# Kernel optimization log

Measured on AMD Instinct MI355X. Metric: run time of the kernel, lower is better.

The kernel has to match this reference:

```python
import jax, jax.numpy as jnp
import numpy as np

P = 0.5  # dropout fraction (init kwarg p)


def setup_inputs() -> dict:
    key = jax.random.key(0)
    # positive weights (e.g. post-softmax attention), shape [B, M, N]
    w = jax.random.uniform(key, (8192, 1, 4096), dtype=jnp.float32, minval=1e-4, maxval=1.0)
    return {"w": w}


def reference(w) -> jnp.ndarray:
    # Drop the bottom int(N*P) entries along dim 2 (per row), then renormalize
    # the surviving entries with a softmax over them; dropped entries stay 0.
    B, M, N = w.shape
    k = int(N * P)  # number of smallest entries zeroed per row
    if k == 0:
        return w
    order = jnp.argsort(w, axis=2)          # ascending order indices
    ranks = jnp.argsort(order, axis=2)      # rank of each element in its row
    keep = ranks >= k                        # True for the top (N-k) entries
    neg = jnp.finfo(w.dtype).min
    logits = jnp.where(keep, w, neg)
    m = jnp.max(logits, axis=2, keepdims=True)
    e = jnp.where(keep, jnp.exp(logits - m), 0.0)
    return e / jnp.sum(e, axis=2, keepdims=True)
```

## Files before the change

kernel.cpp:

```cpp
#include <hip/hip_runtime.h>
#include <stdint.h>

constexpr int N     = 4096;
constexpr int KSEL  = 2048;
constexpr int BLOCK = 256;
constexpr int NW    = BLOCK / 64;
constexpr int EPT   = N / BLOCK;
constexpr int NB    = 256;
constexpr int CAP   = 128;
constexpr float P1  = 0.45f;
constexpr float P2  = 0.55f;
constexpr float BSCALE = 2560.0f;

typedef float vfloat4 __attribute__((ext_vector_type(4)));

__global__ __launch_bounds__(BLOCK, 8)
void wdrop_kernel(const float* __restrict__ w, float* __restrict__ out) {
    const int t = threadIdx.x, wid = t >> 6, lane = t & 63;
    const uint64_t row = blockIdx.x;

    __shared__ alignas(16) int hist[NB];
    __shared__ uint32_t redu[NW];
    __shared__ int      redi[NW];
    __shared__ float    redf[NW];
    __shared__ int      selb, selc, cn;
    __shared__ uint32_t cb[CAP];
    __shared__ int      ci[CAP];
    __shared__ uint32_t thrT, thrI;

    uint32_t v[EPT];
    {
        const uint4* wf = (const uint4*)(w + row * N);
        uint4 u[EPT / 4];
#pragma unroll
        for (int j = 0; j < EPT / 4; ++j) u[j] = wf[j * BLOCK + t];
#pragma unroll
        for (int j = 0; j < EPT / 4; ++j) {
            v[j*4+0] = u[j].x; v[j*4+1] = u[j].y;
            v[j*4+2] = u[j].z; v[j*4+3] = u[j].w;
        }
    }
    hist[t] = 0;
    if (t == 0) cn = 0;

    uint32_t mx = v[0];
    int clo = 0, chi = 0;
#pragma unroll
    for (int e = 0; e < EPT; ++e) {
        mx = max(mx, v[e]);
        const float f = __uint_as_float(v[e]);
        clo += (f < P1); chi += (f < P2);
    }
    int pk = (clo << 16) | chi;
#pragma unroll
    for (int off = 32; off > 0; off >>= 1) {
        mx = max(mx, (uint32_t)__shfl_xor((int)mx, off, 64));
        pk += __shfl_xor(pk, off, 64);
    }
    if (lane == 0) { redu[wid] = mx; redi[wid] = pk; }
    __syncthreads();

#pragma unroll
    for (int e = 0; e < EPT; ++e) {
        const float f = __uint_as_float(v[e]);
        if (f >= P1 && f < P2) {
            const int bk = min((int)((f - P1) * BSCALE), NB - 1);
            atomicAdd(&hist[bk], 1);
        }
    }
    uint32_t mxb = redu[0]; int pkt = redi[0];
#pragma unroll
    for (int i = 1; i < NW; ++i) { mxb = max(mxb, redu[i]); pkt += redi[i]; }
    const int cloB = pkt >> 16, chiB = pkt & 0xFFFF;
    const bool fastp = (cloB < KSEL) && (chiB >= KSEL);
    const int jrank = KSEL - cloB;
    __syncthreads();

    if (wid == 0) {
        const int4 hh = ((const int4*)hist)[lane];
        const int a0 = hh.x, a1 = a0 + hh.y, a2 = a1 + hh.z, a3 = a2 + hh.w;
        int sc = a3;
#pragma unroll
        for (int off = 1; off < 64; off <<= 1) {
            const int u = __shfl_up(sc, off, 64);
            if (lane >= off) sc += u;
        }
        const int base = sc - a3;
        if (fastp) {
            const int inc[4] = {base + a0, base + a1, base + a2, base + a3};
            const int exc[4] = {base, base + a0, base + a1, base + a2};
#pragma unroll
            for (int i = 0; i < 4; ++i)
                if (exc[i] < jrank && jrank <= inc[i]) { selb = lane * 4 + i; selc = exc[i]; }
        }
    }
    __syncthreads();

    if (fastp) {
        const int bs = selb;
#pragma unroll
        for (int e = 0; e < EPT; ++e) {
            const float f = __uint_as_float(v[e]);
            if (f >= P1 && f < P2 && min((int)((f - P1) * BSCALE), NB - 1) == bs) {
                const int slot = atomicAdd(&cn, 1);
                if (slot < CAP) {
                    cb[slot] = v[e];
                    ci[slot] = ((e >> 2) * BLOCK + t) * 4 + (e & 3);
                }
            }
        }
    }
    __syncthreads();

    const bool ok = fastp && (cn <= CAP);
    if (ok && t < cn) {
        const uint32_t myb = cb[t]; const int myi = ci[t];
        const int cc = cn;
        int rank = 0;
        for (int q = 0; q < cc; ++q)
            rank += (cb[q] < myb) || (cb[q] == myb && ci[q] < myi);
        if (rank == jrank - selc - 1) { thrT = myb; thrI = (uint32_t)myi; }
    }

    if (!ok) {
        uint32_t blo = 0u, bhi = 0x7f7fffffu;
        while (blo < bhi) {
            const uint32_t mid = blo + ((bhi - blo) >> 1);
            int c = 0;
#pragma unroll
            for (int e = 0; e < EPT; ++e) c += __popcll(__ballot(v[e] <= mid));
            __syncthreads();
            if (lane == 0) redi[wid] = c;
            __syncthreads();
            int tot = 0;
#pragma unroll
            for (int i = 0; i < NW; ++i) tot += redi[i];
            if (tot >= KSEL) bhi = mid; else blo = mid + 1;
        }
        const uint32_t T = blo;
        int c = 0;
#pragma unroll
        for (int e = 0; e < EPT; ++e) c += __popcll(__ballot(v[e] < T));
        __syncthreads();
        if (lane == 0) redi[wid] = c;
        __syncthreads();
        int clt = 0;
#pragma unroll
        for (int i = 0; i < NW; ++i) clt += redi[i];
        const int need = KSEL - clt;
        int ilo = 0, ihi = N - 1;
        while (ilo < ihi) {
            const int imid = (ilo + ihi) >> 1;
            int cc2 = 0;
#pragma unroll
            for (int e = 0; e < EPT; ++e) {
                const int idx = ((e >> 2) * BLOCK + t) * 4 + (e & 3);
                cc2 += __popcll(__ballot(v[e] == T && idx <= imid));
            }
            __syncthreads();
            if (lane == 0) redi[wid] = cc2;
            __syncthreads();
            int tot = 0;
#pragma unroll
            for (int i = 0; i < NW; ++i) tot += redi[i];
            if (tot >= need) ihi = imid; else ilo = imid + 1;
        }
        if (t == 0) { thrT = T; thrI = (uint32_t)ilo; }
    }
    __syncthreads();

    const uint32_t T = thrT; const int ti = (int)thrI;
    const float m = __uint_as_float(mxb);
    float acc = 0.0f;
#pragma unroll
    for (int e = 0; e < EPT; ++e) {
        const int idx = ((e >> 2) * BLOCK + t) * 4 + (e & 3);
        const bool keep = (v[e] > T) || (v[e] == T && idx > ti);
        const float ev = keep ? __expf(__uint_as_float(v[e]) - m) : 0.0f;
        v[e] = __float_as_uint(ev);
        acc += ev;
    }
#pragma unroll
    for (int off = 32; off > 0; off >>= 1) acc += __shfl_xor(acc, off, 64);
    if (lane == 0) redf[wid] = acc;
    __syncthreads();
    float s = redf[0];
#pragma unroll
    for (int i = 1; i < NW; ++i) s += redf[i];
    const float inv = 1.0f / s;

    vfloat4* of = (vfloat4*)(out + row * N);
#pragma unroll
    for (int j = 0; j < EPT / 4; ++j) {
        vfloat4 o;
        o.x = __uint_as_float(v[j*4+0]) * inv;
        o.y = __uint_as_float(v[j*4+1]) * inv;
        o.z = __uint_as_float(v[j*4+2]) * inv;
        o.w = __uint_as_float(v[j*4+3]) * inv;
        __builtin_nontemporal_store(o, &of[j * BLOCK + t]);
    }
}

extern "C" void kernel_launch(void* const* d_in, const int* in_sizes, int n_in,
                              void* d_out, int out_size, void* d_ws, size_t ws_size,
                              hipStream_t stream) {
    const float* w = (const float*)d_in[0];
    float* out = (float*)d_out;
    const int rows = in_sizes[0] / N;
    wdrop_kernel<<<rows, BLOCK, 0, stream>>>(w, out);
}
```

Baseline: 232.0 us.

## Map one row per wavefront and drop block-level synchronisation

Each wavefront now processes a whole row with 64 elements per lane, using per-wave histograms, ballot-based candidate compaction and shuffle reductions instead of block-wide barriers and shared reductions. The max pass is removed and exp is applied to raw values, relying on softmax shift invariance. This removes barrier and shared-memory reduction overhead, at the cost of higher register pressure, lower occupancy and overflow risk for large inputs.

```diff
diff --git a/kernel.cpp b/kernel.cpp
--- a/kernel.cpp
+++ b/kernel.cpp
@@ -4,200 +4,174 @@
 constexpr int N     = 4096;
 constexpr int KSEL  = 2048;
 constexpr int BLOCK = 256;
-constexpr int NW    = BLOCK / 64;
-constexpr int EPT   = N / BLOCK;
+constexpr int NWAVE = BLOCK / 64;
+constexpr int EPL   = 64;
 constexpr int NB    = 256;
-constexpr int CAP   = 128;
+constexpr int CAP   = 64;
 constexpr float P1  = 0.45f;
 constexpr float P2  = 0.55f;
 constexpr float BSCALE = 2560.0f;
 
 typedef float vfloat4 __attribute__((ext_vector_type(4)));
 
-__global__ __launch_bounds__(BLOCK, 8)
+__global__ __launch_bounds__(BLOCK, 4)
 void wdrop_kernel(const float* __restrict__ w, float* __restrict__ out) {
     const int t = threadIdx.x, wid = t >> 6, lane = t & 63;
-    const uint64_t row = blockIdx.x;
+    const uint64_t row = (uint64_t)blockIdx.x * NWAVE + wid;
 
-    __shared__ alignas(16) int hist[NB];
-    __shared__ uint32_t redu[NW];
-    __shared__ int      redi[NW];
-    __shared__ float    redf[NW];
-    __shared__ int      selb, selc, cn;
-    __shared__ uint32_t cb[CAP];
-    __shared__ int      ci[CAP];
-    __shared__ uint32_t thrT, thrI;
+    __shared__ alignas(16) int hist[NWAVE][NB];
+    __shared__ uint32_t cb[NWAVE][CAP];
+    __shared__ int      ci[NWAVE][CAP];
 
-    uint32_t v[EPT];
+    uint32_t v[EPL];
     {
         const uint4* wf = (const uint4*)(w + row * N);
-        uint4 u[EPT / 4];
+        uint4 u[16];
 #pragma unroll
-        for (int j = 0; j < EPT / 4; ++j) u[j] = wf[j * BLOCK + t];
+        for (int j = 0; j < 16; ++j) u[j] = wf[j * 64 + lane];
 #pragma unroll
-        for (int j = 0; j < EPT / 4; ++j) {
+        for (int j = 0; j < 16; ++j) {
             v[j*4+0] = u[j].x; v[j*4+1] = u[j].y;
             v[j*4+2] = u[j].z; v[j*4+3] = u[j].w;
         }
     }
-    hist[t] = 0;
-    if (t == 0) cn = 0;
 
-    uint32_t mx = v[0];
-    int clo = 0, chi = 0;
+    ((int4*)hist[wid])[lane] = int4{0, 0, 0, 0};
+    __threadfence_block();
+
+    int clo = 0;
 #pragma unroll
-    for (int e = 0; e < EPT; ++e) {
-        mx = max(mx, v[e]);
+    for (int e = 0; e < EPL; ++e) {
         const float f = __uint_as_float(v[e]);
-        clo += (f < P1); chi += (f < P2);
+        clo += (f < P1);
+        if (f >= P1 && f < P2)
+            atomicAdd(&hist[wid][min((int)((f - P1) * BSCALE), NB - 1)], 1);
     }
-    int pk = (clo << 16) | chi;
 #pragma unroll
-    for (int off = 32; off > 0; off >>= 1) {
-        mx = max(mx, (uint32_t)__shfl_xor((int)mx, off, 64));
-        pk += __shfl_xor(pk, off, 64);
+    for (int off = 32; off > 0; off >>= 1) clo += __shfl_xor(clo, off, 64);
+    __threadfence_block();
+
+    const int4 hh = ((const int4*)hist[wid])[lane];
+    const int a0 = hh.x, a1 = a0 + hh.y, a2 = a1 + hh.z, a3 = a2 + hh.w;
+    int sc = a3;
+#pragma unroll
+    for (int off = 1; off < 64; off <<= 1) {
+        const int u = __shfl_up(sc, off, 64);
+        if (lane >= off) sc += u;
     }
-    if (lane == 0) { redu[wid] = mx; redi[wid] = pk; }
-    __syncthreads();
+    const int base = sc - a3;
+    const int tot  = __shfl(sc, 63, 64);
+    bool fastp = (clo < KSEL) && (clo + tot >= KSEL);
+    int selb = -1, jms = 0;
+    if (fastp) {
+        const int jrank = KSEL - clo;
+        const int inc[4] = {base + a0, base + a1, base + a2, base + a3};
+        const int exc[4] = {base, base + a0, base + a1, base + a2};
+#pragma unroll
+        for (int i = 0; i < 4; ++i)
+            if (exc[i] < jrank && jrank <= inc[i]) {
+                selb = lane * 4 + i;
+                jms  = jrank - exc[i] - 1;
+            }
+        const unsigned long long b = __ballot(selb >= 0);
+        const int src = __ffsll((unsigned long long)b) - 1;
+        selb = __shfl(selb, src, 64);
+        jms  = __shfl(jms,  src, 64);
+    }
 
+    uint32_t thrT = 0; int thrI = 0;
+    if (fastp) {
+        int cn = 0;
 #pragma unroll
-    for (int e = 0; e < EPT; ++e) {
-        const float f = __uint_as_float(v[e]);
-        if (f >= P1 && f < P2) {
-            const int bk = min((int)((f - P1) * BSCALE), NB - 1);
-            atomicAdd(&hist[bk], 1);
+        for (int e = 0; e < EPL; ++e) {
+            const float f = __uint_as_float(v[e]);
+            const bool in = (f >= P1) && (f < P2) &&
+                            (min((int)((f - P1) * BSCALE), NB - 1) == selb);
+            const unsigned long long m = __ballot(in);
+            if (in) {
+                const int slot = cn + __popcll(m & ((1ull << lane) - 1ull));
+                if (slot < CAP) {
+                    cb[wid][slot] = v[e];
+                    ci[wid][slot] = ((e >> 2) * 64 + lane) * 4 + (e & 3);
+                }
+            }
+            cn += __popcll(m);
+        }
+        if (cn > CAP) fastp = false;
+        if (fastp) {
+            __threadfence_block();
+            bool found = false; uint32_t myT = 0; int myI = 0;
+            if (lane < cn) {
+                const uint32_t myb = cb[wid][lane]; const int myi = ci[wid][lane];
+                int rank = 0;
+                for (int q = 0; q < cn; ++q)
+                    rank += (cb[wid][q] < myb) ||
+                            (cb[wid][q] == myb && ci[wid][q] < myi);
+                if (rank == jms) { found = true; myT = myb; myI = myi; }
+            }
+            const unsigned long long b = __ballot(found);
+            const int src = __ffsll((unsigned long long)b) - 1;
+            thrT = (uint32_t)__shfl((int)myT, src, 64);
+            thrI = __shfl(myI, src, 64);
         }
     }
-    uint32_t mxb = redu[0]; int pkt = redi[0];
-#pragma unroll
-    for (int i = 1; i < NW; ++i) { mxb = max(mxb, redu[i]); pkt += redi[i]; }
-    const int cloB = pkt >> 16, chiB = pkt & 0xFFFF;
-    const bool fastp = (cloB < KSEL) && (chiB >= KSEL);
-    const int jrank = KSEL - cloB;
-    __syncthreads();
 
-    if (wid == 0) {
-        const int4 hh = ((const int4*)hist)[lane];
-        const int a0 = hh.x, a1 = a0 + hh.y, a2 = a1 + hh.z, a3 = a2 + hh.w;
-        int sc = a3;
-#pragma unroll
-        for (int off = 1; off < 64; off <<= 1) {
-            const int u = __shfl_up(sc, off, 64);
-            if (lane >= off) sc += u;
-        }
-        const int base = sc - a3;
-        if (fastp) {
-            const int inc[4] = {base + a0, base + a1, base + a2, base + a3};
-            const int exc[4] = {base, base + a0, base + a1, base + a2};
-#pragma unroll
-            for (int i = 0; i < 4; ++i)
-                if (exc[i] < jrank && jrank <= inc[i]) { selb = lane * 4 + i; selc = exc[i]; }
-        }
-    }
-    __syncthreads();
-
-    if (fastp) {
-        const int bs = selb;
-#pragma unroll
-        for (int e = 0; e < EPT; ++e) {
-            const float f = __uint_as_float(v[e]);
-            if (f >= P1 && f < P2 && min((int)((f - P1) * BSCALE), NB - 1) == bs) {
-                const int slot = atomicAdd(&cn, 1);
-                if (slot < CAP) {
-                    cb[slot] = v[e];
-                    ci[slot] = ((e >> 2) * BLOCK + t) * 4 + (e & 3);
-                }
-            }
-        }
-    }
-    __syncthreads();
-
-    const bool ok = fastp && (cn <= CAP);
-    if (ok && t < cn) {
-        const uint32_t myb = cb[t]; const int myi = ci[t];
-        const int cc = cn;
-        int rank = 0;
-        for (int q = 0; q < cc; ++q)
-            rank += (cb[q] < myb) || (cb[q] == myb && ci[q] < myi);
-        if (rank == jrank - selc - 1) { thrT = myb; thrI = (uint32_t)myi; }
-    }
-
-    if (!ok) {
+    if (!fastp) {
         uint32_t blo = 0u, bhi = 0x7f7fffffu;
         while (blo < bhi) {
             const uint32_t mid = blo + ((bhi - blo) >> 1);
             int c = 0;
 #pragma unroll
-            for (int e = 0; e < EPT; ++e) c += __popcll(__ballot(v[e] <= mid));
-            __syncthreads();
-            if (lane == 0) redi[wid] = c;
-            __syncthreads();
-            int tot = 0;
+            for (int e = 0; e < EPL; ++e) c += (v[e] <= mid);
 #pragma unroll
-            for (int i = 0; i < NW; ++i) tot += redi[i];
-            if (tot >= KSEL) bhi = mid; else blo = mid + 1;
+            for (int off = 32; off > 0; off >>= 1) c += __shfl_xor(c, off, 64);
+            if (c >= KSEL) bhi = mid; else blo = mid + 1;
         }
         const uint32_t T = blo;
         int c = 0;
 #pragma unroll
-        for (int e = 0; e < EPT; ++e) c += __popcll(__ballot(v[e] < T));
-        __syncthreads();
-        if (lane == 0) redi[wid] = c;
-        __syncthreads();
-        int clt = 0;
+        for (int e = 0; e < EPL; ++e) c += (v[e] < T);
 #pragma unroll
-        for (int i = 0; i < NW; ++i) clt += redi[i];
-        const int need = KSEL - clt;
+        for (int off = 32; off > 0; off >>= 1) c += __shfl_xor(c, off, 64);
+        const int need = KSEL - c;
         int ilo = 0, ihi = N - 1;
         while (ilo < ihi) {
             const int imid = (ilo + ihi) >> 1;
-            int cc2 = 0;
+            int cc = 0;
 #pragma unroll
-            for (int e = 0; e < EPT; ++e) {
-                const int idx = ((e >> 2) * BLOCK + t) * 4 + (e & 3);
-                cc2 += __popcll(__ballot(v[e] == T && idx <= imid));
+            for (int e = 0; e < EPL; ++e) {
+                const int idx = ((e >> 2) * 64 + lane) * 4 + (e & 3);
+                cc += (v[e] == T && idx <= imid);
             }
-            __syncthreads();
-            if (lane == 0) redi[wid] = cc2;
-            __syncthreads();
-            int tot = 0;
 #pragma unroll
-            for (int i = 0; i < NW; ++i) tot += redi[i];
-            if (tot >= need) ihi = imid; else ilo = imid + 1;
+            for (int off = 32; off > 0; off >>= 1) cc += __shfl_xor(cc, off, 64);
+            if (cc >= need) ihi = imid; else ilo = imid + 1;
         }
-        if (t == 0) { thrT = T; thrI = (uint32_t)ilo; }
+        thrT = T; thrI = ilo;
     }
-    __syncthreads();
 
-    const uint32_t T = thrT; const int ti = (int)thrI;
-    const float m = __uint_as_float(mxb);
     float acc = 0.0f;
 #pragma unroll
-    for (int e = 0; e < EPT; ++e) {
-        const int idx = ((e >> 2) * BLOCK + t) * 4 + (e & 3);
-        const bool keep = (v[e] > T) || (v[e] == T && idx > ti);
-        const float ev = keep ? __expf(__uint_as_float(v[e]) - m) : 0.0f;
+    for (int e = 0; e < EPL; ++e) {
+        const int idx = ((e >> 2) * 64 + lane) * 4 + (e & 3);
+        const bool keep = (v[e] > thrT) || (v[e] == thrT && idx > thrI);
+        const float ev = keep ? __expf(__uint_as_float(v[e])) : 0.0f;
         v[e] = __float_as_uint(ev);
         acc += ev;
     }
 #pragma unroll
     for (int off = 32; off > 0; off >>= 1) acc += __shfl_xor(acc, off, 64);
-    if (lane == 0) redf[wid] = acc;
-    __syncthreads();
-    float s = redf[0];
-#pragma unroll
-    for (int i = 1; i < NW; ++i) s += redf[i];
-    const float inv = 1.0f / s;
+    const float inv = 1.0f / acc;
 
     vfloat4* of = (vfloat4*)(out + row * N);
 #pragma unroll
-    for (int j = 0; j < EPT / 4; ++j) {
+    for (int j = 0; j < 16; ++j) {
         vfloat4 o;
         o.x = __uint_as_float(v[j*4+0]) * inv;
         o.y = __uint_as_float(v[j*4+1]) * inv;
         o.z = __uint_as_float(v[j*4+2]) * inv;
         o.w = __uint_as_float(v[j*4+3]) * inv;
-        __builtin_nontemporal_store(o, &of[j * BLOCK + t]);
+        __builtin_nontemporal_store(o, &of[j * 64 + lane]);
     }
 }
 
@@ -207,5 +181,5 @@
     const float* w = (const float*)d_in[0];
     float* out = (float*)d_out;
     const int rows = in_sizes[0] / N;
-    wdrop_kernel<<<rows, BLOCK, 0, stream>>>(w, out);
+    wdrop_kernel<<<rows / NWAVE, BLOCK, 0, stream>>>(w, out);
 }
```

Result: slower. 241.1 us (+3.9%).

## Single-pass per-wave histogram and candidate pool, drop max reduction

Applied to the files above, without the earlier changes.

Replaces the two-pass selection (global histogram, then a second scan of registers for the selected bucket) with a single pass. Each wave builds its own histogram and a pool of mid-range values with their indices. Wave 0 then finds the threshold bucket, compacts candidates from the pools with ballots, and ranks them, which removes several block-wide barriers. The row-max reduction is also dropped: exp is applied directly to the weights, which relies on inputs being at most 1 so that exp cannot overflow. The fallback path now uses shuffle reductions instead of ballots.

```diff
diff --git a/kernel.cpp b/kernel.cpp
--- a/kernel.cpp
+++ b/kernel.cpp
@@ -5,12 +5,13 @@
 constexpr int KSEL  = 2048;
 constexpr int BLOCK = 256;
 constexpr int NW    = BLOCK / 64;
-constexpr int EPT   = N / BLOCK;
-constexpr int NB    = 256;
-constexpr int CAP   = 128;
+constexpr int EPT   = 16;
+constexpr int NB    = 64;
+constexpr int PCAP  = 160;
+constexpr int CCAP  = 48;
 constexpr float P1  = 0.45f;
 constexpr float P2  = 0.55f;
-constexpr float BSCALE = 2560.0f;
+constexpr float BSCALE = 640.0f;
 
 typedef float vfloat4 __attribute__((ext_vector_type(4)));
 
@@ -19,164 +20,168 @@
     const int t = threadIdx.x, wid = t >> 6, lane = t & 63;
     const uint64_t row = blockIdx.x;
 
-    __shared__ alignas(16) int hist[NB];
-    __shared__ uint32_t redu[NW];
+    __shared__ int      hist[NW][NB];
+    __shared__ int      pcnt[NW];
+    __shared__ uint2    pool[NW][PCAP];
+    __shared__ int      wclo[NW];
     __shared__ int      redi[NW];
     __shared__ float    redf[NW];
-    __shared__ int      selb, selc, cn;
-    __shared__ uint32_t cb[CAP];
-    __shared__ int      ci[CAP];
-    __shared__ uint32_t thrT, thrI;
+    __shared__ uint32_t candB[CCAP];
+    __shared__ int      candI[CCAP];
+    __shared__ uint32_t bT, bI;
+    __shared__ int      bFlag;
 
     uint32_t v[EPT];
     {
         const uint4* wf = (const uint4*)(w + row * N);
-        uint4 u[EPT / 4];
-#pragma unroll
-        for (int j = 0; j < EPT / 4; ++j) u[j] = wf[j * BLOCK + t];
-#pragma unroll
-        for (int j = 0; j < EPT / 4; ++j) {
+        uint4 u[4];
+#pragma unroll
+        for (int j = 0; j < 4; ++j) u[j] = wf[j * BLOCK + t];
+#pragma unroll
+        for (int j = 0; j < 4; ++j) {
             v[j*4+0] = u[j].x; v[j*4+1] = u[j].y;
             v[j*4+2] = u[j].z; v[j*4+3] = u[j].w;
         }
     }
-    hist[t] = 0;
-    if (t == 0) cn = 0;
-
-    uint32_t mx = v[0];
-    int clo = 0, chi = 0;
-#pragma unroll
-    for (int e = 0; e < EPT; ++e) {
-        mx = max(mx, v[e]);
-        const float f = __uint_as_float(v[e]);
-        clo += (f < P1); chi += (f < P2);
-    }
-    int pk = (clo << 16) | chi;
-#pragma unroll
-    for (int off = 32; off > 0; off >>= 1) {
-        mx = max(mx, (uint32_t)__shfl_xor((int)mx, off, 64));
-        pk += __shfl_xor(pk, off, 64);
-    }
-    if (lane == 0) { redu[wid] = mx; redi[wid] = pk; }
-    __syncthreads();
-
+
+    hist[wid][lane] = 0;
+    if (lane == 0) pcnt[wid] = 0;
+    __threadfence_block();
+
+    int clo = 0;
 #pragma unroll
     for (int e = 0; e < EPT; ++e) {
         const float f = __uint_as_float(v[e]);
-        if (f >= P1 && f < P2) {
+        if (f < P1) {
+            ++clo;
+        } else if (f < P2) {
             const int bk = min((int)((f - P1) * BSCALE), NB - 1);
-            atomicAdd(&hist[bk], 1);
-        }
-    }
-    uint32_t mxb = redu[0]; int pkt = redi[0];
-#pragma unroll
-    for (int i = 1; i < NW; ++i) { mxb = max(mxb, redu[i]); pkt += redi[i]; }
-    const int cloB = pkt >> 16, chiB = pkt & 0xFFFF;
-    const bool fastp = (cloB < KSEL) && (chiB >= KSEL);
-    const int jrank = KSEL - cloB;
+            atomicAdd(&hist[wid][bk], 1);
+            const int slot = atomicAdd(&pcnt[wid], 1);
+            if (slot < PCAP)
+                pool[wid][slot] = make_uint2(
+                    v[e], (uint32_t)(((e >> 2) * BLOCK + t) * 4 + (e & 3)));
+        }
+    }
+#pragma unroll
+    for (int off = 32; off > 0; off >>= 1) clo += __shfl_xor(clo, off, 64);
+    if (lane == 0) wclo[wid] = clo;
     __syncthreads();
 
     if (wid == 0) {
-        const int4 hh = ((const int4*)hist)[lane];
-        const int a0 = hh.x, a1 = a0 + hh.y, a2 = a1 + hh.z, a3 = a2 + hh.w;
-        int sc = a3;
+        const int cloB = wclo[0] + wclo[1] + wclo[2] + wclo[3];
+        const int h = hist[0][lane] + hist[1][lane] + hist[2][lane] + hist[3][lane];
+        int sc = h;
 #pragma unroll
         for (int off = 1; off < 64; off <<= 1) {
             const int u = __shfl_up(sc, off, 64);
             if (lane >= off) sc += u;
         }
-        const int base = sc - a3;
-        if (fastp) {
-            const int inc[4] = {base + a0, base + a1, base + a2, base + a3};
-            const int exc[4] = {base, base + a0, base + a1, base + a2};
-#pragma unroll
-            for (int i = 0; i < 4; ++i)
-                if (exc[i] < jrank && jrank <= inc[i]) { selb = lane * 4 + i; selc = exc[i]; }
-        }
-    }
-    __syncthreads();
-
-    if (fastp) {
-        const int bs = selb;
-#pragma unroll
-        for (int e = 0; e < EPT; ++e) {
-            const float f = __uint_as_float(v[e]);
-            if (f >= P1 && f < P2 && min((int)((f - P1) * BSCALE), NB - 1) == bs) {
-                const int slot = atomicAdd(&cn, 1);
-                if (slot < CAP) {
-                    cb[slot] = v[e];
-                    ci[slot] = ((e >> 2) * BLOCK + t) * 4 + (e & 3);
+        const int tot = __shfl(sc, 63, 64);
+        bool ok = (cloB < KSEL) && (cloB + tot >= KSEL) &&
+                  (pcnt[0] <= PCAP) && (pcnt[1] <= PCAP) &&
+                  (pcnt[2] <= PCAP) && (pcnt[3] <= PCAP);
+        int selb = -1, jms = 0;
+        if (ok) {
+            const int jrank = KSEL - cloB;
+            const int exc = sc - h;
+            const bool hit = (exc < jrank) && (jrank <= sc);
+            const unsigned long long bb = __ballot(hit);
+            const int src = __ffsll(bb) - 1;
+            selb = __shfl(lane, src, 64);
+            jms  = __shfl(jrank - exc - 1, src, 64);
+        }
+        int cn = 0;
+        if (ok) {
+#pragma unroll
+            for (int wv = 0; wv < NW; ++wv) {
+                const int pn = pcnt[wv];
+                for (int k = 0; k < pn; k += 64) {
+                    const int id = k + lane;
+                    bool in = false; uint2 pe = make_uint2(0u, 0u);
+                    if (id < pn) {
+                        pe = pool[wv][id];
+                        const float pf = __uint_as_float(pe.x);
+                        in = (min((int)((pf - P1) * BSCALE), NB - 1) == selb);
+                    }
+                    const unsigned long long m = __ballot(in);
+                    if (in) {
+                        const int slot = cn + __popcll(m & ((1ull << lane) - 1ull));
+                        if (slot < CCAP) { candB[slot] = pe.x; candI[slot] = (int)pe.y; }
+                    }
+                    cn += __popcll(m);
                 }
             }
-        }
+            if (cn > CCAP) ok = false;
+        }
+        if (ok) {
+            __threadfence_block();
+            if (lane < cn) {
+                const uint32_t myb = candB[lane]; const int myi = candI[lane];
+                int rank = 0;
+                for (int q = 0; q < cn; ++q)
+                    rank += (candB[q] < myb) || (candB[q] == myb && candI[q] < myi);
+                if (rank == jms) { bT = myb; bI = (uint32_t)myi; }
+            }
+        }
+        if (lane == 0) bFlag = ok ? 0 : 1;
     }
     __syncthreads();
 
-    const bool ok = fastp && (cn <= CAP);
-    if (ok && t < cn) {
-        const uint32_t myb = cb[t]; const int myi = ci[t];
-        const int cc = cn;
-        int rank = 0;
-        for (int q = 0; q < cc; ++q)
-            rank += (cb[q] < myb) || (cb[q] == myb && ci[q] < myi);
-        if (rank == jrank - selc - 1) { thrT = myb; thrI = (uint32_t)myi; }
-    }
-
-    if (!ok) {
+    if (bFlag) {
         uint32_t blo = 0u, bhi = 0x7f7fffffu;
         while (blo < bhi) {
             const uint32_t mid = blo + ((bhi - blo) >> 1);
             int c = 0;
 #pragma unroll
-            for (int e = 0; e < EPT; ++e) c += __popcll(__ballot(v[e] <= mid));
-            __syncthreads();
+            for (int e = 0; e < EPT; ++e) c += (v[e] <= mid);
+#pragma unroll
+            for (int off = 32; off > 0; off >>= 1) c += __shfl_xor(c, off, 64);
             if (lane == 0) redi[wid] = c;
             __syncthreads();
-            int tot = 0;
-#pragma unroll
-            for (int i = 0; i < NW; ++i) tot += redi[i];
+            const int tot = redi[0] + redi[1] + redi[2] + redi[3];
+            __syncthreads();
             if (tot >= KSEL) bhi = mid; else blo = mid + 1;
         }
         const uint32_t T = blo;
         int c = 0;
 #pragma unroll
-        for (int e = 0; e < EPT; ++e) c += __popcll(__ballot(v[e] < T));
-        __syncthreads();
+        for (int e = 0; e < EPT; ++e) c += (v[e] < T);
+#pragma unroll
+        for (int off = 32; off > 0; off >>= 1) c += __shfl_xor(c, off, 64);
         if (lane == 0) redi[wid] = c;
         __syncthreads();
-        int clt = 0;
-#pragma unroll
-        for (int i = 0; i < NW; ++i) clt += redi[i];
+        const int clt = redi[0] + redi[1] + redi[2] + redi[3];
+        __syncthreads();
         const int need = KSEL - clt;
         int ilo = 0, ihi = N - 1;
         while (ilo < ihi) {
             const int imid = (ilo + ihi) >> 1;
-            int cc2 = 0;
+            int cc = 0;
 #pragma unroll
             for (int e = 0; e < EPT; ++e) {
                 const int idx = ((e >> 2) * BLOCK + t) * 4 + (e & 3);
-                cc2 += __popcll(__ballot(v[e] == T && idx <= imid));
+                cc += (v[e] == T && idx <= imid);
             }
-            __syncthreads();
-            if (lane == 0) redi[wid] = cc2;
-            __syncthreads();
-            int tot = 0;
-#pragma unroll
-            for (int i = 0; i < NW; ++i) tot += redi[i];
+#pragma unroll
+            for (int off = 32; off > 0; off >>= 1) cc += __shfl_xor(cc, off, 64);
+            if (lane == 0) redi[wid] = cc;
+            __syncthreads();
+            const int tot = redi[0] + redi[1] + redi[2] + redi[3];
+            __syncthreads();
             if (tot >= need) ihi = imid; else ilo = imid + 1;
         }
-        if (t == 0) { thrT = T; thrI = (uint32_t)ilo; }
-    }
-    __syncthreads();
-
-    const uint32_t T = thrT; const int ti = (int)thrI;
-    const float m = __uint_as_float(mxb);
+        if (t == 0) { bT = T; bI = (uint32_t)ilo; }
+        __syncthreads();
+    }
+
+    const uint32_t T = bT; const int ti = (int)bI;
     float acc = 0.0f;
 #pragma unroll
     for (int e = 0; e < EPT; ++e) {
         const int idx = ((e >> 2) * BLOCK + t) * 4 + (e & 3);
         const bool keep = (v[e] > T) || (v[e] == T && idx > ti);
-        const float ev = keep ? __expf(__uint_as_float(v[e]) - m) : 0.0f;
+        const float ev = keep ? __expf(__uint_as_float(v[e])) : 0.0f;
         v[e] = __float_as_uint(ev);
         acc += ev;
     }
@@ -184,20 +189,17 @@
     for (int off = 32; off > 0; off >>= 1) acc += __shfl_xor(acc, off, 64);
     if (lane == 0) redf[wid] = acc;
     __syncthreads();
-    float s = redf[0];
-#pragma unroll
-    for (int i = 1; i < NW; ++i) s += redf[i];
-    const float inv = 1.0f / s;
+    const float inv = 1.0f / (redf[0] + redf[1] + redf[2] + redf[3]);
 
     vfloat4* of = (vfloat4*)(out + row * N);
 #pragma unroll
-    for (int j = 0; j < EPT / 4; ++j) {
+    for (int j = 0; j < 4; ++j) {
         vfloat4 o;
         o.x = __uint_as_float(v[j*4+0]) * inv;
         o.y = __uint_as_float(v[j*4+1]) * inv;
         o.z = __uint_as_float(v[j*4+2]) * inv;
         o.w = __uint_as_float(v[j*4+3]) * inv;
-        __builtin_nontemporal_store(o, &of[j * BLOCK + t]);
+        __builtin_nontemporal_store(o, &((vfloat4*)of)[j * BLOCK + t]);
     }
 }
 
```

After: 232.1 us. No clear change (+0.0%).
